# Kernel tuning notes

Measured on AMD Instinct MI355X. Metric: run time of the kernel, lower is better.

Reference implementation:

```python
import jax, jax.numpy as jnp
import numpy as np
import math

B, S, H, NH = 2, 1024, 768, 12
DH = H // NH  # 64

def setup_inputs() -> dict:
    key = jax.random.key(0)
    ks = jax.random.split(key, 8)
    sc = 0.02
    return {
        "hidden_states": jax.random.normal(ks[0], (B, S, H), jnp.float32),
        "bbox_pos_emb": jax.random.normal(ks[1], (S, S, B, DH), jnp.float32),
        "attention_mask": jnp.zeros((B, 1, 1, S), jnp.float32),
        "Wq": jax.random.normal(ks[2], (H, H), jnp.float32) * sc,
        "bq": jnp.zeros((H,), jnp.float32),
        "Wk": jax.random.normal(ks[3], (H, H), jnp.float32) * sc,
        "bk": jnp.zeros((H,), jnp.float32),
        "Wv": jax.random.normal(ks[4], (H, H), jnp.float32) * sc,
        "bv": jnp.zeros((H,), jnp.float32),
    }

def reference(hidden_states, bbox_pos_emb, attention_mask, Wq, bq, Wk, bk, Wv, bv):
    b, s, h = hidden_states.shape
    def proj(W, bias):
        # (b, s, h) -> (b, nh, s, dh)
        y = hidden_states @ W.T + bias
        return y.reshape(b, s, NH, DH).transpose(0, 2, 1, 3)
    q = proj(Wq, bq)
    k = proj(Wk, bk)
    v = proj(Wv, bv)
    # QK^T: (b, nh, s, s)
    scores = jnp.einsum("bnid,bnjd->bnij", q, k)
    # bbox bias: (s, s, b, dh) -> (b, s, s, dh); bnid,bijd->bnij
    bbox = bbox_pos_emb.transpose(2, 0, 1, 3)
    scores = scores + jnp.einsum("bnid,bijd->bnij", q, bbox)
    scores = scores / math.sqrt(DH)
    scores = scores + attention_mask
    probs = jax.nn.softmax(scores, axis=-1)
    ctx = jnp.einsum("bnij,bnjd->bnid", probs, v)
    ctx = ctx.transpose(0, 2, 1, 3).reshape(b, s, h)
    return ctx
```

## Files before the change

### kernel.cpp

```cpp
#include <hip/hip_runtime.h>
#include <hip/hip_bf16.h>

typedef short bf4 __attribute__((ext_vector_type(4)));
typedef short short8 __attribute__((ext_vector_type(8)));
typedef float f32x4 __attribute__((ext_vector_type(4)));

#define MFMA(a, b, c) __builtin_amdgcn_mfma_f32_16x16x32_bf16((a), (b), (c), 0, 0, 0)

#define NB 2
#define NS 1024
#define NHID 768
#define NHEAD 12
#define NDH 64

__device__ __forceinline__ short f2bf(float x) {
    __hip_bfloat16 h = __float2bfloat16(x);
    return *reinterpret_cast<short*>(&h);
}

typedef const __attribute__((address_space(1))) void gas_t;
typedef __attribute__((address_space(3))) void las_t;
__device__ __forceinline__ void gld_lds16(const float* g, float* l) {
    __builtin_amdgcn_global_load_lds((gas_t*)g, (las_t*)l, 16, 0, 0);
}
__device__ __forceinline__ void gld_lds16s(const short* g, short* l) {
    __builtin_amdgcn_global_load_lds((gas_t*)g, (las_t*)l, 16, 0, 0);
}

#define NHE (2048 * 768)
#define WE  (768 * 768)
__global__ void cvt_bf16_all(
    const float* __restrict__ hidden,
    const float* __restrict__ Wq, const float* __restrict__ Wk,
    const float* __restrict__ Wv,
    short* __restrict__ Xbf, short* __restrict__ Wbf)
{
    const int base = (blockIdx.x * 256 + threadIdx.x) * 4;
    const float* src; short* dst; int off;
    if (base < NHE)               { src = hidden; dst = Xbf;          off = base; }
    else if (base < NHE + WE)     { src = Wq;     dst = Wbf;          off = base - NHE; }
    else if (base < NHE + 2 * WE) { src = Wk;     dst = Wbf + WE;     off = base - NHE - WE; }
    else                          { src = Wv;     dst = Wbf + 2 * WE; off = base - NHE - 2 * WE; }
    f32x4 v = *reinterpret_cast<const f32x4*>(src + off);
    bf4 r;
    r[0] = f2bf(v[0]); r[1] = f2bf(v[1]); r[2] = f2bf(v[2]); r[3] = f2bf(v[3]);
    *reinterpret_cast<bf4*>(dst + off) = r;
}

__global__ __launch_bounds__(256, 3) void qkv_gemm(
    const short* __restrict__ Xbf, const short* __restrict__ Wbf,
    const float* __restrict__ bq, const float* __restrict__ bk,
    const float* __restrict__ bv,
    short* __restrict__ Qo, short* __restrict__ Ko, short* __restrict__ VTo)
{
    const int lane = threadIdx.x & 63;
    const int wave = threadIdx.x >> 6;
    const int lg = lane >> 4, lr = lane & 15;

    const int m0 = blockIdx.x * 128;
    const int n0 = blockIdx.y * 64;
    const int proj = n0 / NHID;
    const int ncol0 = n0 % NHID;
    const float* bias = proj == 0 ? bq : (proj == 1 ? bk : bv);

    __shared__ short Alds[2][128 * 64];
    __shared__ short Blds[2][64 * 64];

    f32x4 acc[2][4];
    #pragma unroll
    for (int mm = 0; mm < 2; ++mm)
        #pragma unroll
        for (int s = 0; s < 4; ++s) acc[mm][s] = (f32x4){0.f, 0.f, 0.f, 0.f};

    auto stage = [&](int t, int buf) {
        const int k0 = t * 64;
        #pragma unroll
        for (int p = 0; p < 4; ++p) {
            const int op = wave * 4 + p;
            const int unit = op * 64 + lane;
            const int r = unit >> 3, u = unit & 7;
            const int g = u ^ (r & 7);
            gld_lds16s(Xbf + (size_t)(m0 + r) * NHID + k0 + g * 8,
                       &Alds[buf][op * 512]);
        }
        #pragma unroll
        for (int p = 0; p < 2; ++p) {
            const int op = wave * 2 + p;
            const int unit = op * 64 + lane;
            const int r = unit >> 3, u = unit & 7;
            const int g = u ^ (r & 7);
            gld_lds16s(Wbf + (size_t)(n0 + r) * NHID + k0 + g * 8,
                       &Blds[buf][op * 512]);
        }
    };

    auto compute = [&](int buf) {
        #pragma unroll
        for (int kk = 0; kk < 2; ++kk) {
            const int U = kk * 4 + lg;
            short8 a[2];
            #pragma unroll
            for (int mm = 0; mm < 2; ++mm) {
                const int R = wave * 32 + mm * 16 + lr;
                a[mm] = *reinterpret_cast<const short8*>(
                    &Alds[buf][(R * 8 + (U ^ (R & 7))) * 8]);
            }
            #pragma unroll
            for (int s = 0; s < 4; ++s) {
                const int R = s * 16 + lr;
                short8 b = *reinterpret_cast<const short8*>(
                    &Blds[buf][(R * 8 + (U ^ (R & 7))) * 8]);
                acc[0][s] = MFMA(a[0], b, acc[0][s]);
                acc[1][s] = MFMA(a[1], b, acc[1][s]);
            }
        }
    };

    stage(0, 0);
    #pragma unroll 2
    for (int t = 0; t < 12; ++t) {
        const int buf = t & 1;
        asm volatile("s_waitcnt vmcnt(0)" ::: "memory");
        __syncthreads();
        if (t < 11) stage(t + 1, buf ^ 1);
        compute(buf);
    }

    #pragma unroll
    for (int mm = 0; mm < 2; ++mm) {
        #pragma unroll
        for (int s = 0; s < 4; ++s) {
            const int ncol = ncol0 + s * 16 + lr;
            const float badd = bias[ncol];
            #pragma unroll
            for (int r = 0; r < 4; ++r) {
                const int m = m0 + wave * 32 + mm * 16 + lg * 4 + r;
                const short v16 = f2bf(acc[mm][s][r] + badd);
                if (proj == 0) {
                    Qo[(size_t)m * NHID + ncol] = v16;
                } else if (proj == 1) {
                    Ko[(size_t)m * NHID + ncol] = v16;
                } else {
                    const int b = m >> 10, ss = m & 1023;
                    const int h = ncol >> 6, dd = ncol & 63;
                    VTo[(((size_t)(b * NHEAD + h) * NDH + dd) << 10) + ss] = v16;
                }
            }
        }
    }
}

__global__ __launch_bounds__(256, 2) void bias_gemm(
    const short* __restrict__ Q,
    const float* __restrict__ bbox,
    float* __restrict__ biasO)
{
    const int lane = threadIdx.x & 63;
    const int wave = threadIdx.x >> 6;
    const int lg = lane >> 4, lr = lane & 15;
    const int i = blockIdx.x;
    const int jq = wave * 256;

    __shared__ float lds[4][2][2048];

    short8 qa[2][2];
    #pragma unroll
    for (int b2 = 0; b2 < 2; ++b2)
        #pragma unroll
        for (int kk = 0; kk < 2; ++kk)
            qa[b2][kk] = *reinterpret_cast<const short8*>(
                Q + ((size_t)(b2 * NS) + i) * NHID + lr * 64 + kk * 32 + lg * 8);

    const int r_half = lane >> 5;
    const int u_lin = lane & 31;

    auto stage = [&](int t, int buf) {
        const int j0 = jq + t * 16;
        float* dst = &lds[wave][buf][0];
        #pragma unroll
        for (int w = 0; w < 8; ++w) {
            const int r = 2 * w + r_half;
            const int u = u_lin ^ (r & 7);
            const float* src = bbox + (size_t)(i * NS + j0 + r) * 128 + u * 4;
            gld_lds16(src, dst + w * 256);
        }
    };

    auto compute = [&](int t, int buf) {
        const float* tile = &lds[wave][buf][0];
        const int j0 = jq + t * 16;
        const int x = lr & 7;
        #pragma unroll
        for (int b2 = 0; b2 < 2; ++b2) {
            f32x4 c = (f32x4){0.f, 0.f, 0.f, 0.f};
            #pragma unroll
            for (int kk = 0; kk < 2; ++kk) {
                const int q0 = b2 * 16 + kk * 8 + lg * 2;
                f32x4 ca = *reinterpret_cast<const f32x4*>(tile + (size_t)(lr * 32 + ((q0)     ^ x)) * 4);
                f32x4 cb = *reinterpret_cast<const f32x4*>(tile + (size_t)(lr * 32 + ((q0 + 1) ^ x)) * 4);
                short8 bf;
                bf[0] = f2bf(ca[0]); bf[1] = f2bf(ca[1]); bf[2] = f2bf(ca[2]); bf[3] = f2bf(ca[3]);
                bf[4] = f2bf(cb[0]); bf[5] = f2bf(cb[1]); bf[6] = f2bf(cb[2]); bf[7] = f2bf(cb[3]);
                c = MFMA(qa[b2][kk], bf, c);
            }
            if (lg < 3) {
                #pragma unroll
                for (int r = 0; r < 4; ++r) {
                    const int n = lg * 4 + r;
                    biasO[((size_t)(b2 * NHEAD + n) * NS + i) * NS + j0 + lr] = c[r];
                }
            }
        }
    };

    stage(0, 0);
    for (int t = 0; t < 16; ++t) {
        const int buf = t & 1;
        asm volatile("s_waitcnt lgkmcnt(0)" ::: "memory");
        if (t < 15) stage(t + 1, buf ^ 1);
        if (t == 0 || t == 15) asm volatile("s_waitcnt vmcnt(8)"  ::: "memory");
        else                   asm volatile("s_waitcnt vmcnt(16)" ::: "memory");
        compute(t, buf);
    }
}

__global__ __launch_bounds__(256, 4) void attn2(
    const short* __restrict__ Q,
    const short* __restrict__ K,
    const short* __restrict__ VT,
    const float* __restrict__ biasO,
    const float* __restrict__ mask,
    float* __restrict__ out)
{
    const int lane = threadIdx.x & 63;
    const int wave = threadIdx.x >> 6;
    const int lg = lane >> 4, lr = lane & 15;
    const int i0 = blockIdx.x * 16;
    const int bh = blockIdx.y;
    const int b = bh / NHEAD, h = bh % NHEAD;
    const int jq = wave * 256;

    __shared__ short plds[4][16][40];
    __shared__ float numlds[4][16][68];
    __shared__ float denlds[4][16];

    short8 qa[2];
    #pragma unroll
    for (int kk = 0; kk < 2; ++kk)
        qa[kk] = *reinterpret_cast<const short8*>(
            Q + ((size_t)(b * NS) + i0 + lr) * NHID + h * 64 + kk * 32 + lg * 8);

    f32x4 ctx[4];
    #pragma unroll
    for (int dt = 0; dt < 4; ++dt) ctx[dt] = (f32x4){0.f, 0.f, 0.f, 0.f};
    f32x4 den = (f32x4){0.f, 0.f, 0.f, 0.f};

    #pragma unroll 2
    for (int t = 0; t < 8; ++t) {
        const int j0 = jq + t * 32;
        f32x4 sc[2];
        #pragma unroll
        for (int s = 0; s < 2; ++s) {
            f32x4 c = (f32x4){0.f, 0.f, 0.f, 0.f};
            #pragma unroll
            for (int kk = 0; kk < 2; ++kk) {
                short8 kf = *reinterpret_cast<const short8*>(
                    K + ((size_t)(b * NS) + j0 + s * 16 + lr) * NHID + h * 64 + kk * 32 + lg * 8);
                c = MFMA(qa[kk], kf, c);
            }
            sc[s] = c;
        }
        const float mk0 = mask[b * NS + j0 + lr];
        const float mk1 = mask[b * NS + j0 + 16 + lr];
        #pragma unroll
        for (int s = 0; s < 2; ++s) {
            const float mk = s == 0 ? mk0 : mk1;
            #pragma unroll
            for (int r = 0; r < 4; ++r) {
                const int i = i0 + lg * 4 + r;
                const float bb = biasO[((size_t)(b * NHEAD + h) * NS + i) * NS + j0 + s * 16 + lr];
                sc[s][r] = __expf((sc[s][r] + bb) * 0.125f + mk);
            }
        }
        den += sc[0] + sc[1];

        #pragma unroll
        for (int s = 0; s < 2; ++s)
            #pragma unroll
            for (int r = 0; r < 4; ++r)
                plds[wave][lg * 4 + r][s * 16 + lr] = f2bf(sc[s][r]);
        asm volatile("" ::: "memory");
        short8 pa = *reinterpret_cast<const short8*>(&plds[wave][lr][lg * 8]);
        asm volatile("" ::: "memory");

        #pragma unroll
        for (int dt = 0; dt < 4; ++dt) {
            short8 vf = *reinterpret_cast<const short8*>(
                VT + ((size_t)(b * NHEAD + h) * NDH + dt * 16 + lr) * NS + j0 + lg * 8);
            ctx[dt] = MFMA(pa, vf, ctx[dt]);
        }
    }

    #pragma unroll
    for (int w = 1; w < 16; w <<= 1) {
        f32x4 o;
        #pragma unroll
        for (int r = 0; r < 4; ++r) o[r] = __shfl_xor(den[r], w, 64);
        den += o;
    }

    #pragma unroll
    for (int dt = 0; dt < 4; ++dt)
        #pragma unroll
        for (int r = 0; r < 4; ++r)
            numlds[wave][lg * 4 + r][dt * 16 + lr] = ctx[dt][r];
    if (lr == 0) {
        #pragma unroll
        for (int r = 0; r < 4; ++r) denlds[wave][lg * 4 + r] = den[r];
    }
    __syncthreads();

    const int ti = threadIdx.x >> 4;
    const int tc = (threadIdx.x & 15) * 4;
    f32x4 n = *reinterpret_cast<const f32x4*>(&numlds[0][ti][tc]);
    n += *reinterpret_cast<const f32x4*>(&numlds[1][ti][tc]);
    n += *reinterpret_cast<const f32x4*>(&numlds[2][ti][tc]);
    n += *reinterpret_cast<const f32x4*>(&numlds[3][ti][tc]);
    const float dd = denlds[0][ti] + denlds[1][ti] + denlds[2][ti] + denlds[3][ti];
    const float inv = 1.0f / dd;
    f32x4 o = n * inv;
    *reinterpret_cast<f32x4*>(out + ((size_t)(b * NS) + i0 + ti) * NHID + h * 64 + tc) = o;
}

extern "C" void kernel_launch(void* const* d_in, const int* in_sizes, int n_in,
                              void* d_out, int out_size, void* d_ws, size_t ws_size,
                              hipStream_t stream) {
    (void)in_sizes; (void)n_in; (void)out_size; (void)ws_size;
    const float* hidden = (const float*)d_in[0];
    const float* bbox   = (const float*)d_in[1];
    const float* mask   = (const float*)d_in[2];
    const float* Wq = (const float*)d_in[3]; const float* bq = (const float*)d_in[4];
    const float* Wk = (const float*)d_in[5]; const float* bk = (const float*)d_in[6];
    const float* Wv = (const float*)d_in[7]; const float* bv = (const float*)d_in[8];
    float* out = (float*)d_out;

    char* ws = (char*)d_ws;
    const size_t qkv_bytes = (size_t)NB * NS * NHID * sizeof(short);
    short* Qw  = (short*)ws;
    short* Kw  = (short*)(ws + qkv_bytes);
    short* VTw = (short*)(ws + 2 * qkv_bytes);
    float* biasW = (float*)(ws + 3 * qkv_bytes);
    const size_t bias_bytes = (size_t)NB * NHEAD * NS * NS * sizeof(float);
    short* Xbf = (short*)(ws + 3 * qkv_bytes + bias_bytes);
    short* Wbf = Xbf + (size_t)2048 * NHID;

    const int cvt_total = (NHE + 3 * WE) / 4;
    cvt_bf16_all<<<cvt_total / 256, 256, 0, stream>>>(hidden, Wq, Wk, Wv, Xbf, Wbf);

    dim3 gp(16, 36);
    qkv_gemm<<<gp, 256, 0, stream>>>(Xbf, Wbf, bq, bk, bv, Qw, Kw, VTw);

    bias_gemm<<<NS, 256, 0, stream>>>(Qw, bbox, biasW);

    dim3 ga(NS / 16, NB * NHEAD);
    attn2<<<ga, 256, 0, stream>>>(Qw, Kw, VTw, biasW, mask, out);
}
```

Before: 234.4 us.

## Store bbox bias as bf16 with scale and mask folded, pipeline attention loads

The bias GEMM now applies the 1/sqrt(dh) scale and the attention mask and writes a bf16 bias tensor instead of fp32, halving the bytes written and then re-read by attention. The attention kernel drops the separate mask read and double-buffers its K, V and bias loads in registers so they overlap with the MFMA work. Launch bounds are relaxed to allow more registers per thread. The cost is precision loss from bf16 bias and mask values, and possibly lower occupancy.

```diff
diff --git a/kernel.cpp b/kernel.cpp
--- a/kernel.cpp
+++ b/kernel.cpp
@@ -153,7 +153,8 @@
 __global__ __launch_bounds__(256, 2) void bias_gemm(
     const short* __restrict__ Q,
     const float* __restrict__ bbox,
-    float* __restrict__ biasO)
+    const float* __restrict__ mask,
+    short* __restrict__ biasH)
 {
     const int lane = threadIdx.x & 63;
     const int wave = threadIdx.x >> 6;
@@ -192,6 +193,7 @@
         const int x = lr & 7;
         #pragma unroll
         for (int b2 = 0; b2 < 2; ++b2) {
+            const float mk = mask[b2 * NS + j0 + lr];
             f32x4 c = (f32x4){0.f, 0.f, 0.f, 0.f};
             #pragma unroll
             for (int kk = 0; kk < 2; ++kk) {
@@ -207,7 +209,8 @@
                 #pragma unroll
                 for (int r = 0; r < 4; ++r) {
                     const int n = lg * 4 + r;
-                    biasO[((size_t)(b2 * NHEAD + n) * NS + i) * NS + j0 + lr] = c[r];
+                    biasH[((size_t)(b2 * NHEAD + n) * NS + i) * NS + j0 + lr] =
+                        f2bf(c[r] * 0.125f + mk);
                 }
             }
         }
@@ -224,12 +227,11 @@
     }
 }
 
-__global__ __launch_bounds__(256, 4) void attn2(
+__global__ __launch_bounds__(256, 2) void attn2(
     const short* __restrict__ Q,
     const short* __restrict__ K,
     const short* __restrict__ VT,
-    const float* __restrict__ biasO,
-    const float* __restrict__ mask,
+    const short* __restrict__ biasH,
     float* __restrict__ out)
 {
     const int lane = threadIdx.x & 63;
@@ -250,38 +252,56 @@
         qa[kk] = *reinterpret_cast<const short8*>(
             Q + ((size_t)(b * NS) + i0 + lr) * NHID + h * 64 + kk * 32 + lg * 8);
 
+    const short* Kb = K + (size_t)b * NS * NHID + h * 64;
+    const short* Vb = VT + (size_t)(b * NHEAD + h) * NDH * NS;
+    const short* Bb = biasH + ((size_t)(b * NHEAD + h) * NS + i0) * NS;
+
     f32x4 ctx[4];
     #pragma unroll
     for (int dt = 0; dt < 4; ++dt) ctx[dt] = (f32x4){0.f, 0.f, 0.f, 0.f};
     f32x4 den = (f32x4){0.f, 0.f, 0.f, 0.f};
 
-    #pragma unroll 2
-    for (int t = 0; t < 8; ++t) {
+    short8 kfA[4], vfA[4]; unsigned short bvA[8];
+    short8 kfB[4], vfB[4]; unsigned short bvB[8];
+
+    auto load = [&](int t, short8* kf, short8* vf, unsigned short* bv) {
         const int j0 = jq + t * 32;
+        #pragma unroll
+        for (int s = 0; s < 2; ++s)
+            #pragma unroll
+            for (int kk = 0; kk < 2; ++kk)
+                kf[s * 2 + kk] = *reinterpret_cast<const short8*>(
+                    Kb + (size_t)(j0 + s * 16 + lr) * NHID + kk * 32 + lg * 8);
+        #pragma unroll
+        for (int dt = 0; dt < 4; ++dt)
+            vf[dt] = *reinterpret_cast<const short8*>(
+                Vb + (size_t)(dt * 16 + lr) * NS + j0 + lg * 8);
+        #pragma unroll
+        for (int s = 0; s < 2; ++s)
+            #pragma unroll
+            for (int r = 0; r < 4; ++r)
+                bv[s * 4 + r] = *reinterpret_cast<const unsigned short*>(
+                    Bb + (size_t)(lg * 4 + r) * NS + j0 + s * 16 + lr);
+    };
+
+    auto compute = [&](const short8* kf, const short8* vf, const unsigned short* bv) {
         f32x4 sc[2];
         #pragma unroll
         for (int s = 0; s < 2; ++s) {
             f32x4 c = (f32x4){0.f, 0.f, 0.f, 0.f};
-            #pragma unroll
-            for (int kk = 0; kk < 2; ++kk) {
-                short8 kf = *reinterpret_cast<const short8*>(
-                    K + ((size_t)(b * NS) + j0 + s * 16 + lr) * NHID + h * 64 + kk * 32 + lg * 8);
-                c = MFMA(qa[kk], kf, c);
-            }
+            c = MFMA(qa[0], kf[s * 2 + 0], c);
+            c = MFMA(qa[1], kf[s * 2 + 1], c);
             sc[s] = c;
         }
-        const float mk0 = mask[b * NS + j0 + lr];
-        const float mk1 = mask[b * NS + j0 + 16 + lr];
-        #pragma unroll
-        for (int s = 0; s < 2; ++s) {
-            const float mk = s == 0 ? mk0 : mk1;
+        #pragma unroll
+        for (int s = 0; s < 2; ++s)
             #pragma unroll
             for (int r = 0; r < 4; ++r) {
-                const int i = i0 + lg * 4 + r;
-                const float bb = biasO[((size_t)(b * NHEAD + h) * NS + i) * NS + j0 + s * 16 + lr];
-                sc[s][r] = __expf((sc[s][r] + bb) * 0.125f + mk);
-            }
-        }
+                const unsigned int u = (unsigned int)bv[s * 4 + r] << 16;
+                float bb;
+                __builtin_memcpy(&bb, &u, 4);
+                sc[s][r] = __expf(sc[s][r] * 0.125f + bb);
+            }
         den += sc[0] + sc[1];
 
         #pragma unroll
@@ -294,11 +314,17 @@
         asm volatile("" ::: "memory");
 
         #pragma unroll
-        for (int dt = 0; dt < 4; ++dt) {
-            short8 vf = *reinterpret_cast<const short8*>(
-                VT + ((size_t)(b * NHEAD + h) * NDH + dt * 16 + lr) * NS + j0 + lg * 8);
-            ctx[dt] = MFMA(pa, vf, ctx[dt]);
-        }
+        for (int dt = 0; dt < 4; ++dt) ctx[dt] = MFMA(pa, vf[dt], ctx[dt]);
+    };
+
+    load(0, kfA, vfA, bvA);
+    #pragma unroll
+    for (int tp = 0; tp < 4; ++tp) {
+        const int t = tp * 2;
+        if (t + 1 < 8) load(t + 1, kfB, vfB, bvB);
+        compute(kfA, vfA, bvA);
+        if (t + 2 < 8) load(t + 2, kfA, vfA, bvA);
+        compute(kfB, vfB, bvB);
     }
 
     #pragma unroll
@@ -349,8 +375,8 @@
     short* Qw  = (short*)ws;
     short* Kw  = (short*)(ws + qkv_bytes);
     short* VTw = (short*)(ws + 2 * qkv_bytes);
-    float* biasW = (float*)(ws + 3 * qkv_bytes);
-    const size_t bias_bytes = (size_t)NB * NHEAD * NS * NS * sizeof(float);
+    short* biasH = (short*)(ws + 3 * qkv_bytes);
+    const size_t bias_bytes = (size_t)NB * NHEAD * NS * NS * sizeof(short);
     short* Xbf = (short*)(ws + 3 * qkv_bytes + bias_bytes);
     short* Wbf = Xbf + (size_t)2048 * NHID;
 
@@ -360,8 +386,8 @@
     dim3 gp(16, 36);
     qkv_gemm<<<gp, 256, 0, stream>>>(Xbf, Wbf, bq, bk, bv, Qw, Kw, VTw);
 
-    bias_gemm<<<NS, 256, 0, stream>>>(Qw, bbox, biasW);
+    bias_gemm<<<NS, 256, 0, stream>>>(Qw, bbox, mask, biasH);
 
     dim3 ga(NS / 16, NB * NHEAD);
-    attn2<<<ga, 256, 0, stream>>>(Qw, Kw, VTw, biasW, mask, out);
-}
+    attn2<<<ga, 256, 0, stream>>>(Qw, Kw, VTw, biasH, out);
+}
```

Measured after the change: 223.9 us. 4.5% less time.

## Store bbox bias as bf16 with scale and mask folded, restructure attention with LDS staging

Applied to the files above, without the earlier changes.

The bias kernel now applies the 1/sqrt(dh) scale and the mask itself and writes the bias tensor in bf16 instead of fp32, halving the largest intermediate's write and read traffic. The attention kernel is rewritten so each block covers 64 query rows, one 16-row strip per wave, over the full key range. K, V^T and bias tiles are double-buffered through LDS with async global-to-LDS loads and swizzling, which removes the cross-wave reduction at the end. XCD-aware block swizzling is added to both the QKV GEMM and attention grids. The bf16 bias adds rounding error, and the new attention grid has far fewer blocks with lower occupancy.

```diff
diff --git a/kernel.cpp b/kernel.cpp
--- a/kernel.cpp
+++ b/kernel.cpp
@@ -16,6 +16,10 @@
 __device__ __forceinline__ short f2bf(float x) {
     __hip_bfloat16 h = __float2bfloat16(x);
     return *reinterpret_cast<short*>(&h);
+}
+
+__device__ __forceinline__ int xcd_swz(int orig, int nwg) {
+    return (orig & 7) * (nwg >> 3) + (orig >> 3);
 }
 
 typedef const __attribute__((address_space(1))) void gas_t;
@@ -57,8 +61,9 @@
     const int wave = threadIdx.x >> 6;
     const int lg = lane >> 4, lr = lane & 15;
 
-    const int m0 = blockIdx.x * 128;
-    const int n0 = blockIdx.y * 64;
+    const int wgid = xcd_swz(blockIdx.x, 16 * 36);
+    const int m0 = (wgid / 36) * 128;
+    const int n0 = (wgid % 36) * 64;
     const int proj = n0 / NHID;
     const int ncol0 = n0 % NHID;
     const float* bias = proj == 0 ? bq : (proj == 1 ? bk : bv);
@@ -153,7 +158,8 @@
 __global__ __launch_bounds__(256, 2) void bias_gemm(
     const short* __restrict__ Q,
     const float* __restrict__ bbox,
-    float* __restrict__ biasO)
+    const float* __restrict__ mask,
+    short* __restrict__ biasH)
 {
     const int lane = threadIdx.x & 63;
     const int wave = threadIdx.x >> 6;
@@ -192,6 +198,7 @@
         const int x = lr & 7;
         #pragma unroll
         for (int b2 = 0; b2 < 2; ++b2) {
+            const float mk = mask[b2 * NS + j0 + lr];
             f32x4 c = (f32x4){0.f, 0.f, 0.f, 0.f};
             #pragma unroll
             for (int kk = 0; kk < 2; ++kk) {
@@ -207,7 +214,8 @@
                 #pragma unroll
                 for (int r = 0; r < 4; ++r) {
                     const int n = lg * 4 + r;
-                    biasO[((size_t)(b2 * NHEAD + n) * NS + i) * NS + j0 + lr] = c[r];
+                    biasH[((size_t)(b2 * NHEAD + n) * NS + i) * NS + j0 + lr] =
+                        f2bf(c[r] * 0.125f + mk);
                 }
             }
         }
@@ -224,25 +232,28 @@
     }
 }
 
-__global__ __launch_bounds__(256, 4) void attn2(
+__global__ __launch_bounds__(256, 3) void attn3(
     const short* __restrict__ Q,
     const short* __restrict__ K,
     const short* __restrict__ VT,
-    const float* __restrict__ biasO,
-    const float* __restrict__ mask,
+    const short* __restrict__ biasH,
     float* __restrict__ out)
 {
-    const int lane = threadIdx.x & 63;
-    const int wave = threadIdx.x >> 6;
+    const int tid = threadIdx.x;
+    const int lane = tid & 63;
+    const int wave = tid >> 6;
     const int lg = lane >> 4, lr = lane & 15;
-    const int i0 = blockIdx.x * 16;
-    const int bh = blockIdx.y;
+
+    const int wgid = xcd_swz(blockIdx.x, 24 * 16);
+    const int bh = wgid >> 4;
+    const int ic = wgid & 15;
     const int b = bh / NHEAD, h = bh % NHEAD;
-    const int jq = wave * 256;
-
-    __shared__ short plds[4][16][40];
-    __shared__ float numlds[4][16][68];
-    __shared__ float denlds[4][16];
+    const int i0 = ic * 64 + wave * 16;
+
+    __shared__ short Klds[2][2048];
+    __shared__ short Vlds[2][2048];
+    __shared__ short Blds[2][2048];
+    __shared__ short plds[4][16 * 40];
 
     short8 qa[2];
     #pragma unroll
@@ -250,55 +261,80 @@
         qa[kk] = *reinterpret_cast<const short8*>(
             Q + ((size_t)(b * NS) + i0 + lr) * NHID + h * 64 + kk * 32 + lg * 8);
 
+    const short* Kb = K + (size_t)b * NS * NHID + h * 64;
+    const short* Vb = VT + (size_t)(b * NHEAD + h) * NDH * NS;
+    const short* Bb = biasH + ((size_t)(b * NHEAD + h) * NS + ic * 64) * NS;
+
     f32x4 ctx[4];
     #pragma unroll
     for (int dt = 0; dt < 4; ++dt) ctx[dt] = (f32x4){0.f, 0.f, 0.f, 0.f};
     f32x4 den = (f32x4){0.f, 0.f, 0.f, 0.f};
 
-    #pragma unroll 2
-    for (int t = 0; t < 8; ++t) {
-        const int j0 = jq + t * 32;
+    const int kr = tid >> 3, ku = tid & 7;
+    const int kgu = ku ^ (kr & 7);
+    const int vr = tid >> 2, vu = tid & 3;
+    const int vgu = vu ^ (vr & 3);
+    const int br = tid >> 2, bu = tid & 3;
+
+    auto stage = [&](int t, int buf) {
+        const int j0 = t * 32;
+        gld_lds16s(Kb + (size_t)(j0 + kr) * NHID + kgu * 8, &Klds[buf][tid * 8]);
+        gld_lds16s(Vb + (size_t)vr * NS + j0 + vgu * 8,     &Vlds[buf][tid * 8]);
+        gld_lds16s(Bb + (size_t)br * NS + j0 + bu * 8,      &Blds[buf][tid * 8]);
+    };
+
+    auto compute = [&](int buf) {
         f32x4 sc[2];
         #pragma unroll
         for (int s = 0; s < 2; ++s) {
             f32x4 c = (f32x4){0.f, 0.f, 0.f, 0.f};
             #pragma unroll
             for (int kk = 0; kk < 2; ++kk) {
+                const int R = s * 16 + lr;
+                const int U = kk * 4 + lg;
                 short8 kf = *reinterpret_cast<const short8*>(
-                    K + ((size_t)(b * NS) + j0 + s * 16 + lr) * NHID + h * 64 + kk * 32 + lg * 8);
+                    &Klds[buf][(R * 8 + (U ^ (R & 7))) * 8]);
                 c = MFMA(qa[kk], kf, c);
             }
             sc[s] = c;
         }
-        const float mk0 = mask[b * NS + j0 + lr];
-        const float mk1 = mask[b * NS + j0 + 16 + lr];
-        #pragma unroll
-        for (int s = 0; s < 2; ++s) {
-            const float mk = s == 0 ? mk0 : mk1;
+        #pragma unroll
+        for (int s = 0; s < 2; ++s)
             #pragma unroll
             for (int r = 0; r < 4; ++r) {
-                const int i = i0 + lg * 4 + r;
-                const float bb = biasO[((size_t)(b * NHEAD + h) * NS + i) * NS + j0 + s * 16 + lr];
-                sc[s][r] = __expf((sc[s][r] + bb) * 0.125f + mk);
-            }
-        }
+                const unsigned int u = (unsigned int)(unsigned short)
+                    Blds[buf][wave * 512 + (lg * 4 + r) * 32 + s * 16 + lr] << 16;
+                float bb;
+                __builtin_memcpy(&bb, &u, 4);
+                sc[s][r] = __expf(sc[s][r] * 0.125f + bb);
+            }
         den += sc[0] + sc[1];
 
         #pragma unroll
         for (int s = 0; s < 2; ++s)
             #pragma unroll
             for (int r = 0; r < 4; ++r)
-                plds[wave][lg * 4 + r][s * 16 + lr] = f2bf(sc[s][r]);
+                plds[wave][(lg * 4 + r) * 40 + s * 16 + lr] = f2bf(sc[s][r]);
         asm volatile("" ::: "memory");
-        short8 pa = *reinterpret_cast<const short8*>(&plds[wave][lr][lg * 8]);
+        short8 pa = *reinterpret_cast<const short8*>(&plds[wave][lr * 40 + lg * 8]);
         asm volatile("" ::: "memory");
 
         #pragma unroll
         for (int dt = 0; dt < 4; ++dt) {
+            const int R = dt * 16 + lr;
             short8 vf = *reinterpret_cast<const short8*>(
-                VT + ((size_t)(b * NHEAD + h) * NDH + dt * 16 + lr) * NS + j0 + lg * 8);
+                &Vlds[buf][(R * 4 + (lg ^ (R & 3))) * 8]);
             ctx[dt] = MFMA(pa, vf, ctx[dt]);
         }
+    };
+
+    stage(0, 0);
+    for (int t = 0; t < 32; ++t) {
+        const int buf = t & 1;
+        asm volatile("s_waitcnt vmcnt(0)" ::: "memory");
+        __syncthreads();
+        if (t < 31) stage(t + 1, buf ^ 1);
+        compute(buf);
     }
 
     #pragma unroll
@@ -310,26 +346,14 @@
     }
 
     #pragma unroll
-    for (int dt = 0; dt < 4; ++dt)
-        #pragma unroll
-        for (int r = 0; r < 4; ++r)
-            numlds[wave][lg * 4 + r][dt * 16 + lr] = ctx[dt][r];
-    if (lr == 0) {
-        #pragma unroll
-        for (int r = 0; r < 4; ++r) denlds[wave][lg * 4 + r] = den[r];
-    }
-    __syncthreads();
-
-    const int ti = threadIdx.x >> 4;
-    const int tc = (threadIdx.x & 15) * 4;
-    f32x4 n = *reinterpret_cast<const f32x4*>(&numlds[0][ti][tc]);
-    n += *reinterpret_cast<const f32x4*>(&numlds[1][ti][tc]);
-    n += *reinterpret_cast<const f32x4*>(&numlds[2][ti][tc]);
-    n += *reinterpret_cast<const f32x4*>(&numlds[3][ti][tc]);
-    const float dd = denlds[0][ti] + denlds[1][ti] + denlds[2][ti] + denlds[3][ti];
-    const float inv = 1.0f / dd;
-    f32x4 o = n * inv;
-    *reinterpret_cast<f32x4*>(out + ((size_t)(b * NS) + i0 + ti) * NHID + h * 64 + tc) = o;
+    for (int r = 0; r < 4; ++r) {
+        const float inv = 1.0f / den[r];
+        const int i = i0 + lg * 4 + r;
+        #pragma unroll
+        for (int dt = 0; dt < 4; ++dt)
+            out[((size_t)(b * NS) + i) * NHID + h * 64 + dt * 16 + lr] =
+                ctx[dt][r] * inv;
+    }
 }
 
 extern "C" void kernel_launch(void* const* d_in, const int* in_sizes, int n_in,
@@ -349,19 +373,17 @@
     short* Qw  = (short*)ws;
     short* Kw  = (short*)(ws + qkv_bytes);
     short* VTw = (short*)(ws + 2 * qkv_bytes);
-    float* biasW = (float*)(ws + 3 * qkv_bytes);
-    const size_t bias_bytes = (size_t)NB * NHEAD * NS * NS * sizeof(float);
+    short* biasH = (short*)(ws + 3 * qkv_bytes);
+    const size_t bias_bytes = (size_t)NB * NHEAD * NS * NS * sizeof(short);
     short* Xbf = (short*)(ws + 3 * qkv_bytes + bias_bytes);
     short* Wbf = Xbf + (size_t)2048 * NHID;
 
     const int cvt_total = (NHE + 3 * WE) / 4;
     cvt_bf16_all<<<cvt_total / 256, 256, 0, stream>>>(hidden, Wq, Wk, Wv, Xbf, Wbf);
 
-    dim3 gp(16, 36);
-    qkv_gemm<<<gp, 256, 0, stream>>>(Xbf, Wbf, bq, bk, bv, Qw, Kw, VTw);
-
-    bias_gemm<<<NS, 256, 0, stream>>>(Qw, bbox, biasW);
-
-    dim3 ga(NS / 16, NB * NHEAD);
-    attn2<<<ga, 256, 0, stream>>>(Qw, Kw, VTw, biasW, mask, out);
-}
+    qkv_gemm<<<16 * 36, 256, 0, stream>>>(Xbf, Wbf, bq, bk, bv, Qw, Kw, VTw);
+
+    bias_gemm<<<NS, 256, 0, stream>>>(Qw, bbox, mask, biasH);
+
+    attn3<<<24 * 16, 256, 0, stream>>>(Qw, Kw, VTw, biasH, out);
+}
```

Result: faster. 215.7 us (-8.0%).
